# Kernel tuning notes

Hardware: AMD Instinct MI355X
Metric: run time of the kernel (lower is better)

## Reference

```python
import jax, jax.numpy as jnp
import numpy as np

N = 100000      # num_nodes
E = 640000      # num_edges
R = 64          # num_relations
D = 128         # emb_dim
L = 2           # num_layers


def setup_inputs() -> dict:
    key = jax.random.key(0)
    ks = jax.random.split(key, 24)
    s = 0.05
    inp = {}
    inp['edge_index'] = jax.random.randint(ks[0], (2, E), 0, N, dtype=jnp.int64)
    inp['edge_type'] = jax.random.randint(ks[1], (E,), 0, R, dtype=jnp.int64)
    inp['embed_w'] = jax.random.normal(ks[2], (N, D), jnp.float32) * s
    inp['rel_emb_w'] = jax.random.normal(ks[3], (L, R, D), jnp.float32) * s
    # rel_mlp: Linear(D,2D) ReLU Linear(2D,2D) ReLU Linear(2D,2D) ReLU Linear(2D,2D)   (hidden_layers=3)
    inp['rmw0'] = jax.random.normal(ks[4], (L, 2 * D, D), jnp.float32) * s
    inp['rmb0'] = jnp.zeros((L, 2 * D), jnp.float32)
    inp['rmw1'] = jax.random.normal(ks[5], (L, 2 * D, 2 * D), jnp.float32) * s
    inp['rmb1'] = jnp.zeros((L, 2 * D), jnp.float32)
    inp['rmw2'] = jax.random.normal(ks[6], (L, 2 * D, 2 * D), jnp.float32) * s
    inp['rmb2'] = jnp.zeros((L, 2 * D), jnp.float32)
    inp['rmw3'] = jax.random.normal(ks[7], (L, 2 * D, 2 * D), jnp.float32) * s
    inp['rmb3'] = jnp.zeros((L, 2 * D), jnp.float32)
    # per-edge linear W: Linear(D,D)
    inp['W_w'] = jax.random.normal(ks[8], (L, D, D), jnp.float32) * s
    inp['W_b'] = jnp.zeros((L, D), jnp.float32)
    # node update mlp: Linear(D,2D) ReLU Linear(2D,D)
    inp['mlp_w0'] = jax.random.normal(ks[9], (L, 2 * D, D), jnp.float32) * s
    inp['mlp_b0'] = jnp.zeros((L, 2 * D), jnp.float32)
    inp['mlp_w1'] = jax.random.normal(ks[10], (L, D, 2 * D), jnp.float32) * s
    inp['mlp_b1'] = jnp.zeros((L, D), jnp.float32)
    inp['eps'] = jnp.zeros((L,), jnp.float32)
    return inp


def reference(edge_index, edge_type, embed_w, rel_emb_w,
              rmw0, rmb0, rmw1, rmb1, rmw2, rmb2, rmw3, rmb3,
              W_w, W_b, mlp_w0, mlp_b0, mlp_w1, mlp_b1, eps):
    src = edge_index[0]  # x_j source nodes
    dst = edge_index[1]  # aggregation targets
    x = embed_w  # [N, D]
    for l in range(L):
        # relation FiLM params: compute once per relation id, gather per edge
        h = jax.nn.relu(rel_emb_w[l] @ rmw0[l].T + rmb0[l])
        h = jax.nn.relu(h @ rmw1[l].T + rmb1[l])
        h = jax.nn.relu(h @ rmw2[l].T + rmb2[l])
        gb = h @ rmw3[l].T + rmb3[l]          # [R, 2D]
        gamma, beta = gb[:, :D], gb[:, D:]
        # W x_j : transform all nodes (N < E), then gather per edge
        xw = x @ W_w[l].T + W_b[l]            # [N, D]
        m = gamma[edge_type] * xw[src] + beta[edge_type]  # [E, D]
        aggr = jax.ops.segment_sum(m, dst, num_segments=N)
        out = (1.0 + eps[l]) * x + aggr
        x = jax.nn.relu(out @ mlp_w0[l].T + mlp_b0[l]) @ mlp_w1[l].T + mlp_b1[l]
        # dropout is identity in eval mode
    return x
```

## Files before the change

kernel.cpp:

```cpp
#include <hip/hip_runtime.h>
#include <hip/hip_fp16.h>
#include <stdint.h>

#define N_NODES 100000
#define N_EDGES 640000
#define R_REL   64
#define D_DIM   128
#define L_LAYERS 2

#define SCAN_CHUNK 1024
#define NBLK_SCAN ((N_NODES + SCAN_CHUNK - 1) / SCAN_CHUNK)

#define LDA 136
#define LDT 264
#define MROWS 128
#define GMLP ((N_NODES + MROWS - 1) / MROWS)

typedef __attribute__((ext_vector_type(8))) short   short8;
typedef __attribute__((ext_vector_type(4))) unsigned short ushort4v;
typedef __attribute__((ext_vector_type(4))) float   f32x4;

__device__ __forceinline__ unsigned short f32_to_bf16(float f) {
  union { float f; uint32_t u; } v; v.f = f;
  uint32_t u = v.u;
  u += 0x7fffu + ((u >> 16) & 1u);
  return (unsigned short)(u >> 16);
}
__device__ __forceinline__ unsigned short f2h(float f) {
  __half h = __float2half(f);
  return __half_as_ushort(h);
}
__device__ __forceinline__ __half2 u2h(unsigned int u) {
  union { unsigned int u; __half2 h; } v; v.u = u; return v.h;
}

__global__ __launch_bounds__(256)
void hist_kernel(const int* __restrict__ ei, int* __restrict__ deg) {
  int idx = blockIdx.x * 256 + threadIdx.x;
  atomicAdd(&deg[ei[N_EDGES + idx]], 1);
}

__global__ __launch_bounds__(256)
void scan_part1(const int* __restrict__ deg, int* __restrict__ partial) {
  __shared__ int lds[256];
  const int b = blockIdx.x, t = threadIdx.x;
  const int base = b * SCAN_CHUNK + t * 4;
  int s = 0;
  for (int k = 0; k < 4; ++k) { int i = base + k; s += (i < N_NODES) ? deg[i] : 0; }
  lds[t] = s; __syncthreads();
  for (int off = 128; off > 0; off >>= 1) {
    if (t < off) lds[t] += lds[t + off];
    __syncthreads();
  }
  if (t == 0) partial[b] = lds[0];
}

__global__ __launch_bounds__(128)
void scan_part2(int* __restrict__ partial, int* __restrict__ blockoff) {
  __shared__ int lds[128];
  const int t = threadIdx.x;
  const int v = (t < NBLK_SCAN) ? partial[t] : 0;
  lds[t] = v; __syncthreads();
  for (int off = 1; off < 128; off <<= 1) {
    int add = (t >= off) ? lds[t - off] : 0;
    __syncthreads();
    lds[t] += add;
    __syncthreads();
  }
  if (t < NBLK_SCAN) blockoff[t] = lds[t] - v;
}

__global__ __launch_bounds__(256)
void scan_part3(const int* __restrict__ deg, const int* __restrict__ blockoff,
                int* __restrict__ rowptr, int* __restrict__ cursor) {
  __shared__ int lds[256];
  const int b = blockIdx.x, t = threadIdx.x;
  const int base = b * SCAN_CHUNK + t * 4;
  int v[4]; int s = 0;
  for (int k = 0; k < 4; ++k) {
    int i = base + k;
    v[k] = (i < N_NODES) ? deg[i] : 0;
    s += v[k];
  }
  lds[t] = s; __syncthreads();
  for (int off = 1; off < 256; off <<= 1) {
    int add = (t >= off) ? lds[t - off] : 0;
    __syncthreads();
    lds[t] += add;
    __syncthreads();
  }
  int excl = lds[t] - s + blockoff[b];
  for (int k = 0; k < 4; ++k) {
    int i = base + k;
    if (i < N_NODES) { rowptr[i] = excl; cursor[i] = excl; excl += v[k]; }
  }
  if (b == 0 && t == 0) rowptr[N_NODES] = N_EDGES;
}

__global__ __launch_bounds__(256)
void scatter_kernel(const int* __restrict__ ei, const int* __restrict__ et,
                    int* __restrict__ cursor, int2* __restrict__ edges2) {
  int idx = blockIdx.x * 256 + threadIdx.x;
  int dst = ei[N_EDGES + idx];
  int slot = atomicAdd(&cursor[dst], 1);
  edges2[slot] = make_int2(ei[idx], et[idx]);
}

__global__ __launch_bounds__(256)
void prep_kernel(const float* __restrict__ rel_emb,
                 const float* __restrict__ rmw0, const float* __restrict__ rmb0,
                 const float* __restrict__ rmw1, const float* __restrict__ rmb1,
                 const float* __restrict__ rmw2, const float* __restrict__ rmb2,
                 const float* __restrict__ rmw3, const float* __restrict__ rmb3,
                 unsigned short* __restrict__ gbb,
                 const float* __restrict__ Ww, const float* __restrict__ mw0,
                 const float* __restrict__ mw1,
                 unsigned short* __restrict__ Wwb, unsigned short* __restrict__ mw0b,
                 unsigned short* __restrict__ mw1b) {
  if (blockIdx.x >= 128) {
    int i = (blockIdx.x - 128) * 256 + threadIdx.x;
    if (i < L_LAYERS * D_DIM * D_DIM)     Wwb[i]  = f32_to_bf16(Ww[i]);
    if (i < L_LAYERS * 2 * D_DIM * D_DIM) mw0b[i] = f32_to_bf16(mw0[i]);
    if (i < L_LAYERS * 2 * D_DIM * D_DIM) mw1b[i] = f32_to_bf16(mw1[i]);
    return;
  }
  __shared__ float bufA[2 * D_DIM];
  __shared__ float bufB[2 * D_DIM];
  const int l = blockIdx.x >> 6;
  const int r = blockIdx.x & 63;
  const int j = threadIdx.x;

  if (j < D_DIM) bufA[j] = rel_emb[(l * R_REL + r) * D_DIM + j];
  __syncthreads();
  {
    const float* w = rmw0 + ((size_t)l * 2 * D_DIM + j) * D_DIM;
    float s = rmb0[l * 2 * D_DIM + j];
    for (int k = 0; k < D_DIM; k += 4) {
      float4 wv = *(const float4*)(w + k);
      s += wv.x * bufA[k] + wv.y * bufA[k + 1] + wv.z * bufA[k + 2] + wv.w * bufA[k + 3];
    }
    bufB[j] = fmaxf(s, 0.0f);
  }
  __syncthreads();
  {
    const float* w = rmw1 + ((size_t)l * 2 * D_DIM + j) * 2 * D_DIM;
    float s = rmb1[l * 2 * D_DIM + j];
    for (int k = 0; k < 2 * D_DIM; k += 4) {
      float4 wv = *(const float4*)(w + k);
      s += wv.x * bufB[k] + wv.y * bufB[k + 1] + wv.z * bufB[k + 2] + wv.w * bufB[k + 3];
    }
    __syncthreads();
    bufA[j] = fmaxf(s, 0.0f);
  }
  __syncthreads();
  {
    const float* w = rmw2 + ((size_t)l * 2 * D_DIM + j) * 2 * D_DIM;
    float s = rmb2[l * 2 * D_DIM + j];
    for (int k = 0; k < 2 * D_DIM; k += 4) {
      float4 wv = *(const float4*)(w + k);
      s += wv.x * bufA[k] + wv.y * bufA[k + 1] + wv.z * bufA[k + 2] + wv.w * bufA[k + 3];
    }
    __syncthreads();
    bufB[j] = fmaxf(s, 0.0f);
  }
  __syncthreads();
  {
    const float* w = rmw3 + ((size_t)l * 2 * D_DIM + j) * 2 * D_DIM;
    float s = rmb3[l * 2 * D_DIM + j];
    for (int k = 0; k < 2 * D_DIM; k += 4) {
      float4 wv = *(const float4*)(w + k);
      s += wv.x * bufB[k] + wv.y * bufB[k + 1] + wv.z * bufB[k + 2] + wv.w * bufB[k + 3];
    }
    const int t = l * R_REL + r;
    if (j < D_DIM) {
      gbb[t * 256 + (j >> 1) * 4 + (j & 1)] = f2h(s);
    } else {
      int c = j - D_DIM;
      gbb[t * 256 + (c >> 1) * 4 + 2 + (c & 1)] = f2h(s);
    }
  }
}

__global__ __launch_bounds__(256)
void xw_kernel(const float* __restrict__ x,
               const unsigned short* __restrict__ Wwb,
               const float* __restrict__ Wb,
               unsigned short* __restrict__ xwb) {
  __shared__ unsigned short a_lds[32 * LDA];
  const int tid = threadIdx.x;
  const int m0 = blockIdx.x * 32;

  for (int i = tid; i < 1024; i += 256) {
    int row = i >> 5, ch = i & 31;
    float4 v = *(const float4*)&x[(m0 + row) * D_DIM + ch * 4];
    ushort4v s;
    s[0] = f32_to_bf16(v.x); s[1] = f32_to_bf16(v.y);
    s[2] = f32_to_bf16(v.z); s[3] = f32_to_bf16(v.w);
    *(ushort4v*)&a_lds[row * LDA + ch * 4] = s;
  }
  __syncthreads();

  const int wave = tid >> 6, lane = tid & 63;
  const int lrow = lane & 15, quad = lane >> 4;
  const int n0 = wave * 32;

  f32x4 acc[2][2] = {};
  for (int ks = 0; ks < 128; ks += 32) {
    short8 a0 = *(const short8*)&a_lds[lrow * LDA + ks + quad * 8];
    short8 a1 = *(const short8*)&a_lds[(16 + lrow) * LDA + ks + quad * 8];
    short8 b0 = *(const short8*)&Wwb[(n0 + lrow) * D_DIM + ks + quad * 8];
    short8 b1 = *(const short8*)&Wwb[(n0 + 16 + lrow) * D_DIM + ks + quad * 8];
    acc[0][0] = __builtin_amdgcn_mfma_f32_16x16x32_bf16(a0, b0, acc[0][0], 0, 0, 0);
    acc[0][1] = __builtin_amdgcn_mfma_f32_16x16x32_bf16(a0, b1, acc[0][1], 0, 0, 0);
    acc[1][0] = __builtin_amdgcn_mfma_f32_16x16x32_bf16(a1, b0, acc[1][0], 0, 0, 0);
    acc[1][1] = __builtin_amdgcn_mfma_f32_16x16x32_bf16(a1, b1, acc[1][1], 0, 0, 0);
  }

  for (int mt = 0; mt < 2; ++mt)
    for (int nt = 0; nt < 2; ++nt)
      for (int rr = 0; rr < 4; ++rr) {
        int row = mt * 16 + quad * 4 + rr;
        int col = n0 + nt * 16 + lrow;
        xwb[(size_t)(m0 + row) * D_DIM + col] = f2h(acc[mt][nt][rr] + Wb[col]);
      }
}

__global__ __launch_bounds__(256)
void agg_kernel(const int2* __restrict__ edges2, const int* __restrict__ rowptr,
                const float* __restrict__ x, const unsigned short* __restrict__ xwb,
                const unsigned short* __restrict__ gbt, const float* __restrict__ eps,
                unsigned short* __restrict__ o) {
  const int lane = threadIdx.x & 63;
  const int n = __builtin_amdgcn_readfirstlane(blockIdx.x * 4 + (threadIdx.x >> 6));
  const int beg = rowptr[n], end = rowptr[n + 1];

  float acc0 = 0.0f, acc1 = 0.0f;
  int e = beg;
  for (; e + 2 <= end; e += 2) {
    int2 ed0 = edges2[e];
    int2 ed1 = edges2[e + 1];
    __half2 xa = *(const __half2*)&xwb[(size_t)ed0.x * D_DIM + lane * 2];
    __half2 xb = *(const __half2*)&xwb[(size_t)ed1.x * D_DIM + lane * 2];
    uint2 ga = *(const uint2*)&gbt[ed0.y * 256 + lane * 4];
    uint2 gb = *(const uint2*)&gbt[ed1.y * 256 + lane * 4];
    __half2 m0 = __hfma2(u2h(ga.x), xa, u2h(ga.y));
    __half2 m1 = __hfma2(u2h(gb.x), xb, u2h(gb.y));
    float2 f0 = __half22float2(m0);
    float2 f1 = __half22float2(m1);
    acc0 += f0.x + f1.x;
    acc1 += f0.y + f1.y;
  }
  if (e < end) {
    int2 ed0 = edges2[e];
    __half2 xa = *(const __half2*)&xwb[(size_t)ed0.x * D_DIM + lane * 2];
    uint2 ga = *(const uint2*)&gbt[ed0.y * 256 + lane * 4];
    __half2 m0 = __hfma2(u2h(ga.x), xa, u2h(ga.y));
    float2 f0 = __half22float2(m0);
    acc0 += f0.x;
    acc1 += f0.y;
  }

  const float e1v = 1.0f + eps[0];
  float2 xr = *(const float2*)&x[(size_t)n * D_DIM + lane * 2];
  unsigned int w = (unsigned int)f32_to_bf16(e1v * xr.x + acc0)
                 | ((unsigned int)f32_to_bf16(e1v * xr.y + acc1) << 16);
  *(unsigned int*)&o[(size_t)n * D_DIM + lane * 2] = w;
}

__global__ __launch_bounds__(512, 4)
void mlp_kernel(const unsigned short* __restrict__ o,
                const unsigned short* __restrict__ w0b, const float* __restrict__ b0,
                const unsigned short* __restrict__ w1b, const float* __restrict__ b1,
                float* __restrict__ y,
                const unsigned short* __restrict__ WwNb,
                const float* __restrict__ WbN,
                unsigned short* __restrict__ xwbN) {
  __shared__ unsigned short u_lds[MROWS * LDT];
  unsigned short* a_lds = u_lds;
  unsigned short* t_lds = u_lds;

  const int tid = threadIdx.x;
  const int m0 = blockIdx.x * MROWS;

  for (int i = tid; i < MROWS * 16; i += 512) {
    int row = i >> 4, seg = i & 15;
    int rg = m0 + row; if (rg >= N_NODES) rg = N_NODES - 1;
    *(short8*)&a_lds[row * LDA + seg * 8] =
        *(const short8*)&o[(size_t)rg * D_DIM + seg * 8];
  }
  __syncthreads();

  const int wave = tid >> 6, lane = tid & 63;
  const int lrow = lane & 15, quad = lane >> 4;

  {
    const int n0 = wave * 32;
    f32x4 acc[8][2] = {};
    #pragma unroll
    for (int ks = 0; ks < 128; ks += 32) {
      short8 bf0 = *(const short8*)&w0b[(n0 + lrow) * D_DIM + ks + quad * 8];
      short8 bf1 = *(const short8*)&w0b[(n0 + 16 + lrow) * D_DIM + ks + quad * 8];
      #pragma unroll
      for (int mt = 0; mt < 8; ++mt) {
        short8 a = *(const short8*)&a_lds[(mt * 16 + lrow) * LDA + ks + quad * 8];
        acc[mt][0] = __builtin_amdgcn_mfma_f32_16x16x32_bf16(a, bf0, acc[mt][0], 0, 0, 0);
        acc[mt][1] = __builtin_amdgcn_mfma_f32_16x16x32_bf16(a, bf1, acc[mt][1], 0, 0, 0);
      }
    }
    __syncthreads();
    #pragma unroll
    for (int mt = 0; mt < 8; ++mt)
      #pragma unroll
      for (int nt = 0; nt < 2; ++nt)
        #pragma unroll
        for (int rr = 0; rr < 4; ++rr) {
          int row = mt * 16 + quad * 4 + rr;
          int col = n0 + nt * 16 + lrow;
          float v = acc[mt][nt][rr] + b0[col];
          t_lds[row * LDT + col] = f32_to_bf16(fmaxf(v, 0.0f));
        }
  }
  __syncthreads();

  {
    const int n0 = wave * 16;
    f32x4 acc[8] = {};
    #pragma unroll
    for (int ks = 0; ks < 256; ks += 32) {
      short8 bf = *(const short8*)&w1b[(n0 + lrow) * 2 * D_DIM + ks + quad * 8];
      #pragma unroll
      for (int mt = 0; mt < 8; ++mt) {
        short8 a = *(const short8*)&t_lds[(mt * 16 + lrow) * LDT + ks + quad * 8];
        acc[mt] = __builtin_amdgcn_mfma_f32_16x16x32_bf16(a, bf, acc[mt], 0, 0, 0);
      }
    }
    #pragma unroll
    for (int mt = 0; mt < 8; ++mt)
      #pragma unroll
      for (int rr = 0; rr < 4; ++rr) {
        int row = mt * 16 + quad * 4 + rr;
        int rg = m0 + row;
        float v = acc[mt][rr] + b1[n0 + lrow];
        acc[mt][rr] = v;
        if (rg < N_NODES) y[(size_t)rg * D_DIM + n0 + lrow] = v;
      }

    if (xwbN) {
      __syncthreads();
      #pragma unroll
      for (int mt = 0; mt < 8; ++mt)
        #pragma unroll
        for (int rr = 0; rr < 4; ++rr) {
          int row = mt * 16 + quad * 4 + rr;
          a_lds[row * LDA + n0 + lrow] = f32_to_bf16(acc[mt][rr]);
        }
    }
  }

  if (xwbN) {
    __syncthreads();
    const int n0 = wave * 16;
    f32x4 acc[8] = {};
    #pragma unroll
    for (int ks = 0; ks < 128; ks += 32) {
      short8 bf = *(const short8*)&WwNb[(n0 + lrow) * D_DIM + ks + quad * 8];
      #pragma unroll
      for (int mt = 0; mt < 8; ++mt) {
        short8 a = *(const short8*)&a_lds[(mt * 16 + lrow) * LDA + ks + quad * 8];
        acc[mt] = __builtin_amdgcn_mfma_f32_16x16x32_bf16(a, bf, acc[mt], 0, 0, 0);
      }
    }
    #pragma unroll
    for (int mt = 0; mt < 8; ++mt)
      #pragma unroll
      for (int rr = 0; rr < 4; ++rr) {
        int row = mt * 16 + quad * 4 + rr;
        int rg = m0 + row;
        if (rg < N_NODES)
          xwbN[(size_t)rg * D_DIM + n0 + lrow] = f2h(acc[mt][rr] + WbN[n0 + lrow]);
      }
  }
}

extern "C" void kernel_launch(void* const* d_in, const int* in_sizes, int n_in,
                              void* d_out, int out_size, void* d_ws, size_t ws_size,
                              hipStream_t stream) {
  const int*   ei      = (const int*)d_in[0];
  const int*   et      = (const int*)d_in[1];
  const float* embed   = (const float*)d_in[2];
  const float* rel_emb = (const float*)d_in[3];
  const float* rmw0 = (const float*)d_in[4];  const float* rmb0 = (const float*)d_in[5];
  const float* rmw1 = (const float*)d_in[6];  const float* rmb1 = (const float*)d_in[7];
  const float* rmw2 = (const float*)d_in[8];  const float* rmb2 = (const float*)d_in[9];
  const float* rmw3 = (const float*)d_in[10]; const float* rmb3 = (const float*)d_in[11];
  const float* Ww   = (const float*)d_in[12]; const float* Wb   = (const float*)d_in[13];
  const float* mw0  = (const float*)d_in[14]; const float* mb0  = (const float*)d_in[15];
  const float* mw1  = (const float*)d_in[16]; const float* mb1  = (const float*)d_in[17];
  const float* eps  = (const float*)d_in[18];
  float* out = (float*)d_out;

  float*          W1   = (float*)d_ws;
  unsigned short* xwb  = (unsigned short*)(W1 + (size_t)N_NODES * D_DIM);
  unsigned short* gbb  = xwb + (size_t)N_NODES * D_DIM;
  unsigned short* Wwb  = gbb + L_LAYERS * R_REL * 256;
  unsigned short* mw0b = Wwb + L_LAYERS * D_DIM * D_DIM;
  unsigned short* mw1b = mw0b + L_LAYERS * 2 * D_DIM * D_DIM;
  int*   deg     = (int*)(mw1b + L_LAYERS * 2 * D_DIM * D_DIM);
  int*   rowptr  = deg + N_NODES;
  int*   cursor  = rowptr + N_NODES + 1;
  int*   partial = cursor + N_NODES;
  int*   blockoff= partial + NBLK_SCAN;
  int2*  edges2  = (int2*)(blockoff + NBLK_SCAN + 1);
  unsigned short* obuf = (unsigned short*)(edges2 + N_EDGES);

  hipMemsetAsync(deg, 0, N_NODES * sizeof(int), stream);
  hist_kernel<<<N_EDGES / 256, 256, 0, stream>>>(ei, deg);
  scan_part1<<<NBLK_SCAN, 256, 0, stream>>>(deg, partial);
  scan_part2<<<1, 128, 0, stream>>>(partial, blockoff);
  scan_part3<<<NBLK_SCAN, 256, 0, stream>>>(deg, blockoff, rowptr, cursor);
  scatter_kernel<<<N_EDGES / 256, 256, 0, stream>>>(ei, et, cursor, edges2);
  prep_kernel<<<384, 256, 0, stream>>>(rel_emb, rmw0, rmb0, rmw1, rmb1,
                                       rmw2, rmb2, rmw3, rmb3, gbb,
                                       Ww, mw0, mw1, Wwb, mw0b, mw1b);

  const int gN = N_NODES / 32;
  const int gA = N_NODES / 4;

  xw_kernel<<<gN, 256, 0, stream>>>(embed, Wwb, Wb, xwb);
  agg_kernel<<<gA, 256, 0, stream>>>(edges2, rowptr, embed, xwb, gbb, eps, obuf);
  mlp_kernel<<<GMLP, 512, 0, stream>>>(obuf, mw0b, mb0, mw1b, mb1, W1,
                                       Wwb + D_DIM * D_DIM, Wb + D_DIM, xwb);

  agg_kernel<<<gA, 256, 0, stream>>>(edges2, rowptr, W1, xwb,
                                     gbb + R_REL * 256, eps + 1, obuf);
  mlp_kernel<<<GMLP, 512, 0, stream>>>(obuf, mw0b + 2 * D_DIM * D_DIM, mb0 + 2 * D_DIM,
                                       mw1b + 2 * D_DIM * D_DIM, mb1 + D_DIM, out,
                                       nullptr, nullptr, nullptr);
}
```

Before: 436.6 us.

## Merge setup kernels, fold scan stage, unroll aggregation, stage MLP outputs via LDS

The histogram and weight-prep kernels are merged into one launch, and the scatter and first xw GEMM into another. The single-block scan_part2 is folded into scan_part3 by having every block redo the small partial-sum scan. The aggregation loop is unrolled to four edges so more gathers are in flight per iteration. The MLP epilogue now stages fp32 and fp16 outputs in LDS so global stores are coalesced and vectorised. The aim is fewer launches and better memory efficiency, at the cost of redundant scan work in each block and heavier LDS use in the MLP.

```diff
diff --git a/kernel.cpp b/kernel.cpp
--- a/kernel.cpp
+++ b/kernel.cpp
@@ -13,8 +13,12 @@
 
 #define LDA 136
 #define LDT 264
+#define LDFY 132
 #define MROWS 128
 #define GMLP ((N_NODES + MROWS - 1) / MROWS)
+
+#define HIST_BLKS (N_EDGES / 256)
+#define XW_BLKS   (N_NODES / 32)
 
 typedef __attribute__((ext_vector_type(8))) short   short8;
 typedef __attribute__((ext_vector_type(4))) unsigned short ushort4v;
@@ -33,11 +37,93 @@
 __device__ __forceinline__ __half2 u2h(unsigned int u) {
   union { unsigned int u; __half2 h; } v; v.u = u; return v.h;
 }
+__device__ __forceinline__ short8 frag_from_f32(const float* p) {
+  short8 r;
+  #pragma unroll
+  for (int k = 0; k < 8; ++k) r[k] = (short)f32_to_bf16(p[k]);
+  return r;
+}
 
 __global__ __launch_bounds__(256)
-void hist_kernel(const int* __restrict__ ei, int* __restrict__ deg) {
-  int idx = blockIdx.x * 256 + threadIdx.x;
-  atomicAdd(&deg[ei[N_EDGES + idx]], 1);
+void hist_prep_kernel(const int* __restrict__ ei, int* __restrict__ deg,
+                      const float* __restrict__ rel_emb,
+                      const float* __restrict__ rmw0, const float* __restrict__ rmb0,
+                      const float* __restrict__ rmw1, const float* __restrict__ rmb1,
+                      const float* __restrict__ rmw2, const float* __restrict__ rmb2,
+                      const float* __restrict__ rmw3, const float* __restrict__ rmb3,
+                      unsigned short* __restrict__ gbb,
+                      const float* __restrict__ Ww, const float* __restrict__ mw0,
+                      const float* __restrict__ mw1,
+                      unsigned short* __restrict__ Wwb, unsigned short* __restrict__ mw0b,
+                      unsigned short* __restrict__ mw1b) {
+  if (blockIdx.x < HIST_BLKS) {
+    int idx = blockIdx.x * 256 + threadIdx.x;
+    atomicAdd(&deg[ei[N_EDGES + idx]], 1);
+    return;
+  }
+  const int pb = blockIdx.x - HIST_BLKS;
+  if (pb >= 128) {
+    int i = (pb - 128) * 256 + threadIdx.x;
+    if (i < L_LAYERS * D_DIM * D_DIM)     Wwb[i]  = f32_to_bf16(Ww[i]);
+    if (i < L_LAYERS * 2 * D_DIM * D_DIM) mw0b[i] = f32_to_bf16(mw0[i]);
+    if (i < L_LAYERS * 2 * D_DIM * D_DIM) mw1b[i] = f32_to_bf16(mw1[i]);
+    return;
+  }
+  __shared__ float bufA[2 * D_DIM];
+  __shared__ float bufB[2 * D_DIM];
+  const int l = pb >> 6;
+  const int r = pb & 63;
+  const int j = threadIdx.x;
+
+  if (j < D_DIM) bufA[j] = rel_emb[(l * R_REL + r) * D_DIM + j];
+  __syncthreads();
+  {
+    const float* w = rmw0 + ((size_t)l * 2 * D_DIM + j) * D_DIM;
+    float s = rmb0[l * 2 * D_DIM + j];
+    for (int k = 0; k < D_DIM; k += 4) {
+      float4 wv = *(const float4*)(w + k);
+      s += wv.x * bufA[k] + wv.y * bufA[k + 1] + wv.z * bufA[k + 2] + wv.w * bufA[k + 3];
+    }
+    bufB[j] = fmaxf(s, 0.0f);
+  }
+  __syncthreads();
+  {
+    const float* w = rmw1 + ((size_t)l * 2 * D_DIM + j) * 2 * D_DIM;
+    float s = rmb1[l * 2 * D_DIM + j];
+    for (int k = 0; k < 2 * D_DIM; k += 4) {
+      float4 wv = *(const float4*)(w + k);
+      s += wv.x * bufB[k] + wv.y * bufB[k + 1] + wv.z * bufB[k + 2] + wv.w * bufB[k + 3];
+    }
+    __syncthreads();
+    bufA[j] = fmaxf(s, 0.0f);
+  }
+  __syncthreads();
+  {
+    const float* w = rmw2 + ((size_t)l * 2 * D_DIM + j) * 2 * D_DIM;
+    float s = rmb2[l * 2 * D_DIM + j];
+    for (int k = 0; k < 2 * D_DIM; k += 4) {
+      float4 wv = *(const float4*)(w + k);
+      s += wv.x * bufA[k] + wv.y * bufA[k + 1] + wv.z * bufA[k + 2] + wv.w * bufA[k + 3];
+    }
+    __syncthreads();
+    bufB[j] = fmaxf(s, 0.0f);
+  }
+  __syncthreads();
+  {
+    const float* w = rmw3 + ((size_t)l * 2 * D_DIM + j) * 2 * D_DIM;
+    float s = rmb3[l * 2 * D_DIM + j];
+    for (int k = 0; k < 2 * D_DIM; k += 4) {
+      float4 wv = *(const float4*)(w + k);
+      s += wv.x * bufB[k] + wv.y * bufB[k + 1] + wv.z * bufB[k + 2] + wv.w * bufB[k + 3];
+    }
+    const int t = l * R_REL + r;
+    if (j < D_DIM) {
+      gbb[t * 256 + (j >> 1) * 4 + (j & 1)] = f2h(s);
+    } else {
+      int c = j - D_DIM;
+      gbb[t * 256 + (c >> 1) * 4 + 2 + (c & 1)] = f2h(s);
+    }
+  }
 }
 
 __global__ __launch_bounds__(256)
@@ -55,26 +141,23 @@
   if (t == 0) partial[b] = lds[0];
 }
 
-__global__ __launch_bounds__(128)
-void scan_part2(int* __restrict__ partial, int* __restrict__ blockoff) {
-  __shared__ int lds[128];
-  const int t = threadIdx.x;
-  const int v = (t < NBLK_SCAN) ? partial[t] : 0;
-  lds[t] = v; __syncthreads();
-  for (int off = 1; off < 128; off <<= 1) {
-    int add = (t >= off) ? lds[t - off] : 0;
-    __syncthreads();
-    lds[t] += add;
-    __syncthreads();
-  }
-  if (t < NBLK_SCAN) blockoff[t] = lds[t] - v;
-}
-
 __global__ __launch_bounds__(256)
-void scan_part3(const int* __restrict__ deg, const int* __restrict__ blockoff,
-                int* __restrict__ rowptr, int* __restrict__ cursor) {
+void scan_part3b(const int* __restrict__ deg, const int* __restrict__ partial,
+                 int* __restrict__ rowptr, int* __restrict__ cursor) {
+  __shared__ int plds[128];
   __shared__ int lds[256];
   const int b = blockIdx.x, t = threadIdx.x;
+
+  if (t < 128) plds[t] = (t < NBLK_SCAN) ? partial[t] : 0;
+  __syncthreads();
+  for (int off = 1; off < 128; off <<= 1) {
+    int add = (t < 128 && t >= off) ? plds[t - off] : 0;
+    __syncthreads();
+    if (t < 128) plds[t] += add;
+    __syncthreads();
+  }
+  const int blockoff = (b == 0) ? 0 : plds[b - 1];
+
   const int base = b * SCAN_CHUNK + t * 4;
   int v[4]; int s = 0;
   for (int k = 0; k < 4; ++k) {
@@ -89,7 +172,7 @@
     lds[t] += add;
     __syncthreads();
   }
-  int excl = lds[t] - s + blockoff[b];
+  int excl = lds[t] - s + blockoff;
   for (int k = 0; k < 4; ++k) {
     int i = base + k;
     if (i < N_NODES) { rowptr[i] = excl; cursor[i] = excl; excl += v[k]; }
@@ -98,97 +181,22 @@
 }
 
 __global__ __launch_bounds__(256)
-void scatter_kernel(const int* __restrict__ ei, const int* __restrict__ et,
-                    int* __restrict__ cursor, int2* __restrict__ edges2) {
-  int idx = blockIdx.x * 256 + threadIdx.x;
-  int dst = ei[N_EDGES + idx];
-  int slot = atomicAdd(&cursor[dst], 1);
-  edges2[slot] = make_int2(ei[idx], et[idx]);
-}
-
-__global__ __launch_bounds__(256)
-void prep_kernel(const float* __restrict__ rel_emb,
-                 const float* __restrict__ rmw0, const float* __restrict__ rmb0,
-                 const float* __restrict__ rmw1, const float* __restrict__ rmb1,
-                 const float* __restrict__ rmw2, const float* __restrict__ rmb2,
-                 const float* __restrict__ rmw3, const float* __restrict__ rmb3,
-                 unsigned short* __restrict__ gbb,
-                 const float* __restrict__ Ww, const float* __restrict__ mw0,
-                 const float* __restrict__ mw1,
-                 unsigned short* __restrict__ Wwb, unsigned short* __restrict__ mw0b,
-                 unsigned short* __restrict__ mw1b) {
-  if (blockIdx.x >= 128) {
-    int i = (blockIdx.x - 128) * 256 + threadIdx.x;
-    if (i < L_LAYERS * D_DIM * D_DIM)     Wwb[i]  = f32_to_bf16(Ww[i]);
-    if (i < L_LAYERS * 2 * D_DIM * D_DIM) mw0b[i] = f32_to_bf16(mw0[i]);
-    if (i < L_LAYERS * 2 * D_DIM * D_DIM) mw1b[i] = f32_to_bf16(mw1[i]);
+void scatter_xw_kernel(const int* __restrict__ ei, const int* __restrict__ et,
+                       int* __restrict__ cursor, int2* __restrict__ edges2,
+                       const float* __restrict__ x,
+                       const unsigned short* __restrict__ Wwb,
+                       const float* __restrict__ Wb,
+                       unsigned short* __restrict__ xwb) {
+  if (blockIdx.x < HIST_BLKS) {
+    int idx = blockIdx.x * 256 + threadIdx.x;
+    int dst = ei[N_EDGES + idx];
+    int slot = atomicAdd(&cursor[dst], 1);
+    edges2[slot] = make_int2(ei[idx], et[idx]);
     return;
   }
-  __shared__ float bufA[2 * D_DIM];
-  __shared__ float bufB[2 * D_DIM];
-  const int l = blockIdx.x >> 6;
-  const int r = blockIdx.x & 63;
-  const int j = threadIdx.x;
-
-  if (j < D_DIM) bufA[j] = rel_emb[(l * R_REL + r) * D_DIM + j];
-  __syncthreads();
-  {
-    const float* w = rmw0 + ((size_t)l * 2 * D_DIM + j) * D_DIM;
-    float s = rmb0[l * 2 * D_DIM + j];
-    for (int k = 0; k < D_DIM; k += 4) {
-      float4 wv = *(const float4*)(w + k);
-      s += wv.x * bufA[k] + wv.y * bufA[k + 1] + wv.z * bufA[k + 2] + wv.w * bufA[k + 3];
-    }
-    bufB[j] = fmaxf(s, 0.0f);
-  }
-  __syncthreads();
-  {
-    const float* w = rmw1 + ((size_t)l * 2 * D_DIM + j) * 2 * D_DIM;
-    float s = rmb1[l * 2 * D_DIM + j];
-    for (int k = 0; k < 2 * D_DIM; k += 4) {
-      float4 wv = *(const float4*)(w + k);
-      s += wv.x * bufB[k] + wv.y * bufB[k + 1] + wv.z * bufB[k + 2] + wv.w * bufB[k + 3];
-    }
-    __syncthreads();
-    bufA[j] = fmaxf(s, 0.0f);
-  }
-  __syncthreads();
-  {
-    const float* w = rmw2 + ((size_t)l * 2 * D_DIM + j) * 2 * D_DIM;
-    float s = rmb2[l * 2 * D_DIM + j];
-    for (int k = 0; k < 2 * D_DIM; k += 4) {
-      float4 wv = *(const float4*)(w + k);
-      s += wv.x * bufA[k] + wv.y * bufA[k + 1] + wv.z * bufA[k + 2] + wv.w * bufA[k + 3];
-    }
-    __syncthreads();
-    bufB[j] = fmaxf(s, 0.0f);
-  }
-  __syncthreads();
-  {
-    const float* w = rmw3 + ((size_t)l * 2 * D_DIM + j) * 2 * D_DIM;
-    float s = rmb3[l * 2 * D_DIM + j];
-    for (int k = 0; k < 2 * D_DIM; k += 4) {
-      float4 wv = *(const float4*)(w + k);
-      s += wv.x * bufB[k] + wv.y * bufB[k + 1] + wv.z * bufB[k + 2] + wv.w * bufB[k + 3];
-    }
-    const int t = l * R_REL + r;
-    if (j < D_DIM) {
-      gbb[t * 256 + (j >> 1) * 4 + (j & 1)] = f2h(s);
-    } else {
-      int c = j - D_DIM;
-      gbb[t * 256 + (c >> 1) * 4 + 2 + (c & 1)] = f2h(s);
-    }
-  }
-}
-
-__global__ __launch_bounds__(256)
-void xw_kernel(const float* __restrict__ x,
-               const unsigned short* __restrict__ Wwb,
-               const float* __restrict__ Wb,
-               unsigned short* __restrict__ xwb) {
   __shared__ unsigned short a_lds[32 * LDA];
   const int tid = threadIdx.x;
-  const int m0 = blockIdx.x * 32;
+  const int m0 = (blockIdx.x - HIST_BLKS) * 32;
 
   for (int i = tid; i < 1024; i += 256) {
     int row = i >> 5, ch = i & 31;
@@ -236,25 +244,44 @@
 
   float acc0 = 0.0f, acc1 = 0.0f;
   int e = beg;
-  for (; e + 2 <= end; e += 2) {
-    int2 ed0 = edges2[e];
-    int2 ed1 = edges2[e + 1];
-    __half2 xa = *(const __half2*)&xwb[(size_t)ed0.x * D_DIM + lane * 2];
-    __half2 xb = *(const __half2*)&xwb[(size_t)ed1.x * D_DIM + lane * 2];
-    uint2 ga = *(const uint2*)&gbt[ed0.y * 256 + lane * 4];
-    uint2 gb = *(const uint2*)&gbt[ed1.y * 256 + lane * 4];
-    __half2 m0 = __hfma2(u2h(ga.x), xa, u2h(ga.y));
-    __half2 m1 = __hfma2(u2h(gb.x), xb, u2h(gb.y));
-    float2 f0 = __half22float2(m0);
-    float2 f1 = __half22float2(m1);
+  for (; e + 4 <= end; e += 4) {
+    int2 e0 = edges2[e],     e1 = edges2[e + 1];
+    int2 e2 = edges2[e + 2], e3 = edges2[e + 3];
+    __half2 x0 = *(const __half2*)&xwb[(size_t)e0.x * D_DIM + lane * 2];
+    __half2 x1 = *(const __half2*)&xwb[(size_t)e1.x * D_DIM + lane * 2];
+    __half2 x2 = *(const __half2*)&xwb[(size_t)e2.x * D_DIM + lane * 2];
+    __half2 x3 = *(const __half2*)&xwb[(size_t)e3.x * D_DIM + lane * 2];
+    uint2 g0 = *(const uint2*)&gbt[e0.y * 256 + lane * 4];
+    uint2 g1 = *(const uint2*)&gbt[e1.y * 256 + lane * 4];
+    uint2 g2 = *(const uint2*)&gbt[e2.y * 256 + lane * 4];
+    uint2 g3 = *(const uint2*)&gbt[e3.y * 256 + lane * 4];
+    __half2 m0 = __hfma2(u2h(g0.x), x0, u2h(g0.y));
+    __half2 m1 = __hfma2(u2h(g1.x), x1, u2h(g1.y));
+    __half2 m2 = __hfma2(u2h(g2.x), x2, u2h(g2.y));
+    __half2 m3 = __hfma2(u2h(g3.x), x3, u2h(g3.y));
+    float2 f0 = __half22float2(m0), f1 = __half22float2(m1);
+    float2 f2 = __half22float2(m2), f3 = __half22float2(m3);
+    acc0 += (f0.x + f1.x) + (f2.x + f3.x);
+    acc1 += (f0.y + f1.y) + (f2.y + f3.y);
+  }
+  if (e + 2 <= end) {
+    int2 e0 = edges2[e], e1 = edges2[e + 1];
+    __half2 x0 = *(const __half2*)&xwb[(size_t)e0.x * D_DIM + lane * 2];
+    __half2 x1 = *(const __half2*)&xwb[(size_t)e1.x * D_DIM + lane * 2];
+    uint2 g0 = *(const uint2*)&gbt[e0.y * 256 + lane * 4];
+    uint2 g1 = *(const uint2*)&gbt[e1.y * 256 + lane * 4];
+    __half2 m0 = __hfma2(u2h(g0.x), x0, u2h(g0.y));
+    __half2 m1 = __hfma2(u2h(g1.x), x1, u2h(g1.y));
+    float2 f0 = __half22float2(m0), f1 = __half22float2(m1);
     acc0 += f0.x + f1.x;
     acc1 += f0.y + f1.y;
+    e += 2;
   }
   if (e < end) {
-    int2 ed0 = edges2[e];
-    __half2 xa = *(const __half2*)&xwb[(size_t)ed0.x * D_DIM + lane * 2];
-    uint2 ga = *(const uint2*)&gbt[ed0.y * 256 + lane * 4];
-    __half2 m0 = __hfma2(u2h(ga.x), xa, u2h(ga.y));
+    int2 e0 = edges2[e];
+    __half2 x0 = *(const __half2*)&xwb[(size_t)e0.x * D_DIM + lane * 2];
+    uint2 g0 = *(const uint2*)&gbt[e0.y * 256 + lane * 4];
+    __half2 m0 = __hfma2(u2h(g0.x), x0, u2h(g0.y));
     float2 f0 = __half22float2(m0);
     acc0 += f0.x;
     acc1 += f0.y;
@@ -278,6 +305,8 @@
   __shared__ unsigned short u_lds[MROWS * LDT];
   unsigned short* a_lds = u_lds;
   unsigned short* t_lds = u_lds;
+  float*          yf    = (float*)u_lds;
+  unsigned short* xs    = u_lds;
 
   const int tid = threadIdx.x;
   const int m0 = blockIdx.x * MROWS;
@@ -308,17 +337,15 @@
       }
     }
     __syncthreads();
+    float bb0 = b0[n0 + lrow], bb1 = b0[n0 + 16 + lrow];
     #pragma unroll
     for (int mt = 0; mt < 8; ++mt)
       #pragma unroll
-      for (int nt = 0; nt < 2; ++nt)
-        #pragma unroll
-        for (int rr = 0; rr < 4; ++rr) {
-          int row = mt * 16 + quad * 4 + rr;
-          int col = n0 + nt * 16 + lrow;
-          float v = acc[mt][nt][rr] + b0[col];
-          t_lds[row * LDT + col] = f32_to_bf16(fmaxf(v, 0.0f));
-        }
+      for (int rr = 0; rr < 4; ++rr) {
+        int row = mt * 16 + quad * 4 + rr;
+        t_lds[row * LDT + n0 + lrow]      = f32_to_bf16(fmaxf(acc[mt][0][rr] + bb0, 0.0f));
+        t_lds[row * LDT + n0 + 16 + lrow] = f32_to_bf16(fmaxf(acc[mt][1][rr] + bb1, 0.0f));
+      }
   }
   __syncthreads();
 
@@ -334,31 +361,26 @@
         acc[mt] = __builtin_amdgcn_mfma_f32_16x16x32_bf16(a, bf, acc[mt], 0, 0, 0);
       }
     }
+    __syncthreads();
+    float bb = b1[n0 + lrow];
     #pragma unroll
     for (int mt = 0; mt < 8; ++mt)
       #pragma unroll
       for (int rr = 0; rr < 4; ++rr) {
         int row = mt * 16 + quad * 4 + rr;
-        int rg = m0 + row;
-        float v = acc[mt][rr] + b1[n0 + lrow];
-        acc[mt][rr] = v;
-        if (rg < N_NODES) y[(size_t)rg * D_DIM + n0 + lrow] = v;
-      }
-
-    if (xwbN) {
-      __syncthreads();
-      #pragma unroll
-      for (int mt = 0; mt < 8; ++mt)
-        #pragma unroll
-        for (int rr = 0; rr < 4; ++rr) {
-          int row = mt * 16 + quad * 4 + rr;
-          a_lds[row * LDA + n0 + lrow] = f32_to_bf16(acc[mt][rr]);
-        }
-    }
+        yf[row * LDFY + n0 + lrow] = acc[mt][rr] + bb;
+      }
+  }
+  __syncthreads();
+
+  for (int i = tid; i < MROWS * 32; i += 512) {
+    int row = i >> 5, c4 = i & 31;
+    int rg = m0 + row;
+    if (rg < N_NODES)
+      *(float4*)&y[(size_t)rg * D_DIM + c4 * 4] = *(const float4*)&yf[row * LDFY + c4 * 4];
   }
 
   if (xwbN) {
-    __syncthreads();
     const int n0 = wave * 16;
     f32x4 acc[8] = {};
     #pragma unroll
@@ -366,19 +388,26 @@
       short8 bf = *(const short8*)&WwNb[(n0 + lrow) * D_DIM + ks + quad * 8];
       #pragma unroll
       for (int mt = 0; mt < 8; ++mt) {
-        short8 a = *(const short8*)&a_lds[(mt * 16 + lrow) * LDA + ks + quad * 8];
+        short8 a = frag_from_f32(&yf[(mt * 16 + lrow) * LDFY + ks + quad * 8]);
         acc[mt] = __builtin_amdgcn_mfma_f32_16x16x32_bf16(a, bf, acc[mt], 0, 0, 0);
       }
     }
+    __syncthreads();
+    float bb = WbN[n0 + lrow];
     #pragma unroll
     for (int mt = 0; mt < 8; ++mt)
       #pragma unroll
       for (int rr = 0; rr < 4; ++rr) {
         int row = mt * 16 + quad * 4 + rr;
-        int rg = m0 + row;
-        if (rg < N_NODES)
-          xwbN[(size_t)rg * D_DIM + n0 + lrow] = f2h(acc[mt][rr] + WbN[n0 + lrow]);
-      }
+        xs[row * LDA + n0 + lrow] = f2h(acc[mt][rr] + bb);
+      }
+    __syncthreads();
+    for (int i = tid; i < MROWS * 16; i += 512) {
+      int row = i >> 4, seg = i & 15;
+      int rg = m0 + row;
+      if (rg < N_NODES)
+        *(short8*)&xwbN[(size_t)rg * D_DIM + seg * 8] = *(const short8*)&xs[row * LDA + seg * 8];
+    }
   }
 }
 
@@ -409,24 +438,21 @@
   int*   rowptr  = deg + N_NODES;
   int*   cursor  = rowptr + N_NODES + 1;
   int*   partial = cursor + N_NODES;
-  int*   blockoff= partial + NBLK_SCAN;
-  int2*  edges2  = (int2*)(blockoff + NBLK_SCAN + 1);
+  int*   pad0    = partial + NBLK_SCAN;
+  int2*  edges2  = (int2*)(pad0 + NBLK_SCAN + 1);
   unsigned short* obuf = (unsigned short*)(edges2 + N_EDGES);
 
   hipMemsetAsync(deg, 0, N_NODES * sizeof(int), stream);
-  hist_kernel<<<N_EDGES / 256, 256, 0, stream>>>(ei, deg);
+  hist_prep_kernel<<<HIST_BLKS + 384, 256, 0, stream>>>(
+      ei, deg, rel_emb, rmw0, rmb0, rmw1, rmb1, rmw2, rmb2, rmw3, rmb3, gbb,
+      Ww, mw0, mw1, Wwb, mw0b, mw1b);
   scan_part1<<<NBLK_SCAN, 256, 0, stream>>>(deg, partial);
-  scan_part2<<<1, 128, 0, stream>>>(partial, blockoff);
-  scan_part3<<<NBLK_SCAN, 256, 0, stream>>>(deg, blockoff, rowptr, cursor);
-  scatter_kernel<<<N_EDGES / 256, 256, 0, stream>>>(ei, et, cursor, edges2);
-  prep_kernel<<<384, 256, 0, stream>>>(rel_emb, rmw0, rmb0, rmw1, rmb1,
-                                       rmw2, rmb2, rmw3, rmb3, gbb,
-                                       Ww, mw0, mw1, Wwb, mw0b, mw1b);
-
-  const int gN = N_NODES / 32;
+  scan_part3b<<<NBLK_SCAN, 256, 0, stream>>>(deg, partial, rowptr, cursor);
+  scatter_xw_kernel<<<HIST_BLKS + XW_BLKS, 256, 0, stream>>>(
+      ei, et, cursor, edges2, embed, Wwb, Wb, xwb);
+
   const int gA = N_NODES / 4;
 
-  xw_kernel<<<gN, 256, 0, stream>>>(embed, Wwb, Wb, xwb);
   agg_kernel<<<gA, 256, 0, stream>>>(edges2, rowptr, embed, xwb, gbb, eps, obuf);
   mlp_kernel<<<GMLP, 512, 0, stream>>>(obuf, mw0b, mb0, mw1b, mb1, W1,
                                        Wwb + D_DIM * D_DIM, Wb + D_DIM, xwb);
```

New measurement: 414.7 us. 5.0% less time.
